# Kernel tuning notes

Measured on AMD Instinct MI355X. Metric: run time of the kernel, lower is better.

Reference implementation:

```python
import jax, jax.numpy as jnp
import numpy as np

N, WORD, R, NW, MODES = 512, 64, 4, 1, 3
EPS = 1e-6

def setup_inputs() -> dict:
    key = jax.random.key(0)
    k1, k2, k3 = jax.random.split(key, 3)
    B, T, C = 8, 16, 1024
    IFACE = R * WORD + R + NW * WORD + NW + NW * WORD + NW * WORD + R + NW + NW + R * MODES  # 471
    return {
        'controller_output': jax.random.normal(k1, (B, T, C), dtype=jnp.float32),
        'W_if': jax.random.normal(k2, (C, IFACE), dtype=jnp.float32) * 0.02,
        'b_if': jnp.zeros((IFACE,), dtype=jnp.float32),
        'memory0': jax.random.normal(k3, (B, N, WORD), dtype=jnp.float32) * 0.1,
    }

def _content_weights(keys, strengths, memory):
    # keys [B,H,W], memory [B,N,W] -> [B,H,N]
    dots = jnp.einsum('bhw,bnw->bhn', keys, memory)
    knorm = jnp.linalg.norm(keys, axis=-1, keepdims=True)          # [B,H,1]
    mnorm = jnp.linalg.norm(memory, axis=-1)                        # [B,N]
    sim = dots / (knorm * mnorm[:, None, :] + EPS)
    return jax.nn.softmax(strengths[..., None] * sim, axis=-1)

def _allocation(usage):
    # usage [B,N] -> allocation weighting [B,N] (DNC free-list)
    phi = jnp.argsort(usage, axis=-1)                               # ascending usage
    su = jnp.take_along_axis(usage, phi, axis=-1)
    cp = jnp.cumprod(jnp.concatenate([jnp.ones_like(su[:, :1]), su[:, :-1]], axis=-1), axis=-1)
    a_sorted = (1.0 - su) * cp
    inv = jnp.argsort(phi, axis=-1)
    return jnp.take_along_axis(a_sorted, inv, axis=-1)

def _parse(v, B):
    idx = [0]
    def take(n):
        out = v[:, idx[0]:idx[0] + n]; idx[0] += n; return out
    read_keys = take(R * WORD).reshape(B, R, WORD)
    read_str = jax.nn.softplus(take(R))
    write_keys = take(NW * WORD).reshape(B, NW, WORD)
    write_str = jax.nn.softplus(take(NW))
    erase = jax.nn.sigmoid(take(NW * WORD).reshape(B, NW, WORD))
    write_vec = take(NW * WORD).reshape(B, NW, WORD)
    free_g = jax.nn.sigmoid(take(R))
    alloc_g = jax.nn.sigmoid(take(NW))
    write_g = jax.nn.sigmoid(take(NW))
    modes = jax.nn.softmax(take(R * MODES).reshape(B, R, MODES), axis=-1)
    return read_keys, read_str, write_keys, write_str, erase, write_vec, free_g, alloc_g, write_g, modes

def _dnc_forward(controller_output, W_if, b_if, memory0):
    B = controller_output.shape[0]
    iface = jnp.einsum('btc,ci->bti', controller_output, W_if) + b_if   # [B,T,I]
    off_diag = 1.0 - jnp.eye(N, dtype=memory0.dtype)

    read_w0 = jnp.zeros((B, R, N), memory0.dtype)
    usage0 = jnp.zeros((B, N), memory0.dtype)
    link0 = jnp.zeros((B, N, N), memory0.dtype)
    prec0 = jnp.zeros((B, N), memory0.dtype)

    def step(carry, iface_t):
        memory, read_w, usage, link, prec = carry
        (rk, rs, wk, ws, erase, wv, fg, ag, wg, modes) = _parse(iface_t, B)
        # write content addressing on previous memory
        w_content = _content_weights(wk, ws, memory)                 # [B,NW,N]
        alloc = _allocation(usage)                                   # [B,N]
        ww = wg[..., None] * (ag[..., None] * alloc[:, None, :] + (1.0 - ag[..., None]) * w_content)  # [B,NW,N]
        # usage update
        psi = jnp.prod(1.0 - fg[..., None] * read_w, axis=1)         # [B,N]
        ws_all = 1.0 - jnp.prod(1.0 - ww, axis=1)                    # [B,N]
        usage = (usage + ws_all - usage * ws_all) * psi
        # memory erase + write
        keep = jnp.prod(1.0 - ww[:, :, :, None] * erase[:, :, None, :], axis=1)  # [B,N,W]
        add = jnp.einsum('bwn,bwk->bnk', ww, wv)
        memory = memory * keep + add
        # temporal linkage (aggregated over write heads, as in the module)
        ww_sum = jnp.sum(ww, axis=1)                                  # [B,N]
        link = ((1.0 - ww_sum[:, :, None] - ww_sum[:, None, :]) * link
                + ww_sum[:, :, None] * prec[:, None, :]) * off_diag
        prec = (1.0 - jnp.sum(ww_sum, axis=-1, keepdims=True)) * prec + ww_sum
        # read addressing on updated memory
        r_content = _content_weights(rk, rs, memory)                  # [B,R,N]
        fwd = jnp.einsum('bnm,brm->brn', link, read_w)
        bwd = jnp.einsum('bmn,brm->brn', link, read_w)
        read_w = (modes[:, :, 0:1] * bwd + modes[:, :, 1:2] * r_content + modes[:, :, 2:3] * fwd)
        read_words = jnp.einsum('brn,bnw->brw', read_w, memory)       # [B,R,W]
        return (memory, read_w, usage, link, prec), read_words

    carry0 = (memory0, read_w0, usage0, link0, prec0)
    (memory, read_w, usage, link, prec), read_words = jax.lax.scan(step, carry0, jnp.swapaxes(iface, 0, 1))
    read_words = jnp.swapaxes(read_words, 0, 1)                       # [B,T,R,W]
    return read_words

def reference(controller_output, W_if, b_if, memory0):
    return _dnc_forward(controller_output, W_if, b_if, memory0)
```

## Files before the change

### kernel.cpp

```cpp
#include <hip/hip_runtime.h>
#include <math.h>


#define NBATCH 8
#define GPB    32
#define NBLK   (NBATCH*GPB)
#define BS     512
#define NROW   16
#define NTT    16
#define NSLOT  512
#define WRD    64
#define RH     4
#define NIF    471
#define LSTR   520
#define MSTR   65
#define EPSV   1e-6f

#define B_ALO  0
#define B_WM   512
#define B_EN   1536
#define B_SEP  5632
#define B_RWP  5760
#define BATF   13952
#define IFCF   (NBATCH*NTT*NIF)
#define PARF   (NBATCH*BATF)

#define P_ERA 328
#define P_WV  392
#define P_WS  456
#define P_FG  457
#define P_AG  461
#define P_WG  462
#define P_MOD 464
#define P_WKN 476
#define P_RKN 477

__device__ __forceinline__ float sigm(float x){ return 1.f/(1.f+expf(-x)); }
__device__ __forceinline__ float softpl(float x){ return x>0.f ? x+log1pf(expf(-x)) : log1pf(expf(x)); }
__device__ __forceinline__ float red16s(float v){ v+=__shfl_xor(v,1,16); v+=__shfl_xor(v,2,16); v+=__shfl_xor(v,4,16); v+=__shfl_xor(v,8,16); return v; }
__device__ __forceinline__ float red32s(float v){ v+=__shfl_xor(v,1,32); v+=__shfl_xor(v,2,32); v+=__shfl_xor(v,4,32); v+=__shfl_xor(v,8,32); v+=__shfl_xor(v,16,32); return v; }
__device__ __forceinline__ float red32m(float v){ v*=__shfl_xor(v,1,32); v*=__shfl_xor(v,2,32); v*=__shfl_xor(v,4,32); v*=__shfl_xor(v,8,32); v*=__shfl_xor(v,16,32); return v; }
__device__ __forceinline__ float red64s(float v){
  v+=__shfl_xor(v,1); v+=__shfl_xor(v,2); v+=__shfl_xor(v,4);
  v+=__shfl_xor(v,8); v+=__shfl_xor(v,16); v+=__shfl_xor(v,32); return v; }

__device__ __forceinline__ void stg(float* p, float v){
  __hip_atomic_store(p, v, __ATOMIC_RELAXED, __HIP_MEMORY_SCOPE_AGENT);
}
__device__ __forceinline__ float ldc(const float* p){
  return __hip_atomic_load(p, __ATOMIC_RELAXED, __HIP_MEMORY_SCOPE_AGENT);
}
__device__ __forceinline__ void stg2(float* p, float x, float y){
  union { float2 f; unsigned long long u; } v; v.f=make_float2(x,y);
  __hip_atomic_store((unsigned long long*)p, v.u, __ATOMIC_RELAXED, __HIP_MEMORY_SCOPE_AGENT);
}
__device__ __forceinline__ float2 ldc2(const float* p){
  union { float2 f; unsigned long long u; } v;
  v.u=__hip_atomic_load((const unsigned long long*)p, __ATOMIC_RELAXED, __HIP_MEMORY_SCOPE_AGENT);
  return v.f;
}

__device__ __forceinline__ void lbar(unsigned* flg, int b, int g, unsigned gen, int tid){
  asm volatile("s_waitcnt vmcnt(0)" ::: "memory");
  __syncthreads();
  if (tid==0) __hip_atomic_store(flg+b*512+g*16, gen, __ATOMIC_RELAXED, __HIP_MEMORY_SCOPE_AGENT);
  if (tid<GPB){
    while (__hip_atomic_load(flg+b*512+tid*16, __ATOMIC_RELAXED, __HIP_MEMORY_SCOPE_AGENT) < gen)
      __builtin_amdgcn_s_sleep(1);
  }
  __syncthreads();
  asm volatile("" ::: "memory");
}

__global__ void __launch_bounds__(BS)
dnc_kernel(const float* __restrict__ ctrl, const float* __restrict__ wif,
           const float* __restrict__ bif, const float* __restrict__ mem0,
           float* __restrict__ out, float* __restrict__ ws, unsigned* __restrict__ flg)
{
  const int tid = threadIdx.x;
  const int bid = blockIdx.x;
  const int b   = bid & 7;
  const int g   = bid >> 3;
  const int n0  = g * NROW;

  __shared__ __align__(16) float L  [NROW*LSTR];
  __shared__ __align__(16) float LT [NROW*LSTR];
  __shared__ __align__(16) float Mem[NROW*MSTR];
  __shared__ __align__(16) float rwl[RH*NSLOT];
  __shared__ __align__(16) float wwl[NSLOT];
  __shared__ __align__(16) float usagel[NSLOT];
  __shared__ __align__(16) float precl[NSLOT];
  __shared__ __align__(16) float prs[488];
  __shared__ __align__(16) float aux[248];
  float* ern    = aux;
  float* fwdb   = aux+64;
  float* bwdb   = aux+128;
  float* modesA = aux+192;
  float* red    = aux+216;

  for (int i=tid; i<NROW*LSTR; i+=BS){ L[i]=0.f; LT[i]=0.f; }
  for (int i=tid; i<NROW*WRD; i+=BS){
    int r=i>>6, k=i&63;
    Mem[r*MSTR+k] = mem0[(size_t)(b*NSLOT + n0 + r)*WRD + k];
  }
  if (tid<NSLOT){ usagel[tid]=0.f; precl[tid]=0.f; }
  if (g < NTT){
    float* ctrlrow = rwl;
    const float* crow = ctrl + (size_t)(b*NTT+g)*1024;
    for (int i=tid;i<1024;i+=BS) ctrlrow[i]=crow[i];
    __syncthreads();
    if (tid<NIF){
      int j=tid;
      float a0=0.f,a1=0.f,a2=0.f,a3=0.f;
      const float* wp = wif + j;
      for (int c=0;c<1024;c+=4){
        a0 += ctrlrow[c+0]*wp[(size_t)(c+0)*NIF];
        a1 += ctrlrow[c+1]*wp[(size_t)(c+1)*NIF];
        a2 += ctrlrow[c+2]*wp[(size_t)(c+2)*NIF];
        a3 += ctrlrow[c+3]*wp[(size_t)(c+3)*NIF];
      }
      ws[(size_t)(b*NTT+g)*NIF + j] = ((a0+a1)+(a2+a3)) + bif[j];
    }
  }
  __syncthreads();
  for (int i=tid;i<RH*NSLOT;i+=BS) rwl[i]=0.f;

  __syncthreads();
  __builtin_amdgcn_fence(__ATOMIC_RELEASE, "agent");
  if (tid==0) __hip_atomic_store(flg+b*512+g*16, 1u, __ATOMIC_RELAXED, __HIP_MEMORY_SCOPE_AGENT);
  if (tid<GPB){
    while (__hip_atomic_load(flg+b*512+tid*16, __ATOMIC_RELAXED, __HIP_MEMORY_SCOPE_AGENT) < 1u)
      __builtin_amdgcn_s_sleep(1);
  }
  __syncthreads();
  __builtin_amdgcn_fence(__ATOMIC_ACQUIRE, "agent");

  {
    float* qb = ws + IFCF + 0*PARF + b*BATF;
    const float* ifc0 = ws + (size_t)(b*NTT+0)*NIF;
    {
      int row=tid>>5, sub=tid&31;
      float wd=0.f, ms=0.f;
      #pragma unroll
      for (int j=0;j<2;j++){
        int k=sub*2+j; float m=Mem[row*MSTR+k];
        wd += m*ifc0[260+k]; ms += m*m;
      }
      wd=red32s(wd); ms=red32s(ms);
      if (sub==0) stg2(qb+B_WM+2*(n0+row), wd, sqrtf(ms));
    }
    {
      int row=tid>>5, sub=tid&31, n=n0+row;
      float u_n=usagel[n], pr=1.f;
      for (int m=sub;m<NSLOT;m+=32){
        float um=usagel[m];
        if (um<u_n || (um==u_n && m<n)) pr*=um;
      }
      pr=red32m(pr);
      if (sub==0) stg(qb+B_ALO+n, (1.f-u_n)*pr);
    }
  }
  {
    const float* ifc = ws + (size_t)(b*NTT+0)*NIF;
    if (tid<324) prs[tid]=ifc[tid];
    __syncthreads();
    if (tid<4) prs[256+tid]=softpl(prs[256+tid]);
    else if (tid==4) prs[P_WS]=softpl(ifc[324]);
    else if (tid>=8 && tid<12) prs[P_FG+(tid-8)]=sigm(ifc[453+(tid-8)]);
    else if (tid==12) prs[P_AG]=sigm(ifc[457]);
    else if (tid==13) prs[P_WG]=sigm(ifc[458]);
    else if (tid>=16 && tid<20){
      int r=tid-16;
      float x0=ifc[459+r*3],x1=ifc[460+r*3],x2=ifc[461+r*3];
      float mx=fmaxf(x0,fmaxf(x1,x2));
      float e0=expf(x0-mx),e1=expf(x1-mx),e2=expf(x2-mx),s=e0+e1+e2;
      prs[P_MOD+r*3+0]=e0/s; prs[P_MOD+r*3+1]=e1/s; prs[P_MOD+r*3+2]=e2/s;
      modesA[r*3+0]=e0/s; modesA[r*3+1]=e1/s; modesA[r*3+2]=e2/s;
    }
    else if (tid>=64 && tid<128) prs[P_ERA+(tid-64)]=sigm(ifc[325+(tid-64)]);
    else if (tid>=192 && tid<256) prs[P_WV+(tid-192)]=ifc[389+(tid-192)];
    {
      int wv=tid>>6, lane=tid&63;
      if (wv<4){
        float v = (wv==0)? prs[260+lane] : prs[(wv-1)*64+lane];
        v = red64s(v*v);
        if (lane==0) prs[P_WKN+wv]=sqrtf(v);
        if (wv==0){
          float u=prs[192+lane];
          u=red64s(u*u);
          if (lane==0) prs[480]=sqrtf(u);
        }
      }
    }
  }
  lbar(flg, b, g, 2u, tid);

  for (int t=0; t<=NTT; t++){
    const float* pb = ws + IFCF + (t&1)*PARF + b*BATF;
    float*       qb = ws + IFCF + ((t+1)&1)*PARF + b*BATF;
    float* mprev = modesA + 12*((t+1)&1);
    float* mcur  = modesA + 12*(t&1);
    const int row = tid>>5, sub = tid&31;

    float2 en[4]; float2 sep2=make_float2(1.f,1.f); float rwpv=0.f;
    float2 wm=make_float2(0.f,1.f); float al=0.f;
    float2 wk2=make_float2(0.f,0.f);
    if (t>0){
      #pragma unroll
      for (int i=0;i<4;i++) en[i]=ldc2(pb+B_EN+2*(tid+BS*i));
      if (tid<64){ int gp=tid>>1, c=tid&1; sep2=ldc2(pb+B_SEP+gp*4+c*2); }
      if (t>=2 && tid<256) rwpv=ldc(pb+B_RWP+(tid&31)*256+g*8+(tid>>5));
    }
    if (t<NTT){
      wm=ldc2(pb+B_WM+2*tid);
      al=ldc(pb+B_ALO+tid);
    }
    if (t<NTT-1){
      const float* ifn = ws + (size_t)(b*NTT+(t+1))*NIF;
      wk2 = *(const float2*)(ifn+260+sub*2);
    }

    float ewv=0.f;
    if (t<NTT){
      ewv=expf(prs[P_WS]*wm.x/(prs[P_WKN]*wm.y+EPSV));
      wwl[tid]=ewv;
    }
    if (t>0 && tid<64){
      float vx=sep2.x, vy=sep2.y;
      vx+=__shfl_xor(vx,2); vy+=__shfl_xor(vy,2);
      vx+=__shfl_xor(vx,4); vy+=__shfl_xor(vy,4);
      vx+=__shfl_xor(vx,8); vy+=__shfl_xor(vy,8);
      vx+=__shfl_xor(vx,16); vy+=__shfl_xor(vy,16);
      vx+=__shfl_xor(vx,32); vy+=__shfl_xor(vy,32);
      if (tid<2){ red[tid*2]=vx; red[tid*2+1]=vy; }
    }
    __syncthreads();

    float psi=1.f;
    if (t>0){
      float rwv[4];
      #pragma unroll
      for (int i=0;i<4;i++){
        rwv[i] = en[i].y + mprev[i*3+1]*en[i].x/red[i];
        rwl[i*NSLOT+tid] = rwv[i];
      }
      psi=(1.f-prs[P_FG+0]*rwv[0])*(1.f-prs[P_FG+1]*rwv[1])
         *(1.f-prs[P_FG+2]*rwv[2])*(1.f-prs[P_FG+3]*rwv[3]);
    }
    if (t<NTT){ float v=red64s(ewv); if ((tid&63)==0) red[4+(tid>>6)]=v; }
    __syncthreads();

    if (t>0 && tid<256){
      int r=tid>>6, k=tid&63;
      float a=0.f;
      #pragma unroll
      for (int rr=0;rr<4;rr++){
        float4 rv=*(const float4*)&rwl[r*NSLOT+n0+rr*4];
        a += rv.x*Mem[(rr*4+0)*MSTR+k] + rv.y*Mem[(rr*4+1)*MSTR+k]
           + rv.z*Mem[(rr*4+2)*MSTR+k] + rv.w*Mem[(rr*4+3)*MSTR+k];
      }
      stg(qb+B_RWP+g*256+tid, a);
    }
    if (t>=2 && tid<256){
      float s=red32s(rwpv);
      if ((tid&31)==0) out[(size_t)(b*NTT+(t-2))*256 + g*8 + (tid>>5)] = s;
    }
    if (t==NTT) break;
    float wwv;
    {
      const float Sw=red[4]+red[5]+red[6]+red[7]+red[8]+red[9]+red[10]+red[11];
      wwv=prs[P_WG]*(prs[P_AG]*al+(1.f-prs[P_AG])*ewv/Sw);
      wwl[tid]=wwv;
      usagel[tid]=(usagel[tid]+wwv-usagel[tid]*wwv)*psi;
      float v=red64s(wwv);
      if ((tid&63)==0) red[12+(tid>>6)]=v;
    }
    __syncthreads();

    {
      float wn =wwl[n0+row];
      float pmn=precl[n0+row];
      float* Lr = &L[row*LSTR];
      float* Tr = &LT[row*LSTR];
      float fa0=0.f,fa1=0.f,fa2=0.f,fa3=0.f, ba0=0.f,ba1=0.f,ba2=0.f,ba3=0.f;
      #pragma unroll 2
      for (int jj=0;jj<4;jj++){
        int mb=(sub+32*jj)*4;
        float4 wm4=*(float4*)&wwl[mb];
        float4 pm4=*(float4*)&precl[mb];
        float c0=1.f-wn-wm4.x, c1=1.f-wn-wm4.y, c2=1.f-wn-wm4.z, c3=1.f-wn-wm4.w;
        int d=(n0+row)-mb;
        float4 l4=*(float4*)&Lr[mb];
        l4.x=c0*l4.x+wn*pm4.x; l4.y=c1*l4.y+wn*pm4.y;
        l4.z=c2*l4.z+wn*pm4.z; l4.w=c3*l4.w+wn*pm4.w;
        if (d>=0 && d<4) ((float*)&l4)[d]=0.f;
        *(float4*)&Lr[mb]=l4;
        float4 r0=*(const float4*)&rwl[0*NSLOT+mb];
        float4 r1=*(const float4*)&rwl[1*NSLOT+mb];
        float4 r2=*(const float4*)&rwl[2*NSLOT+mb];
        float4 r3=*(const float4*)&rwl[3*NSLOT+mb];
        fa0+=l4.x*r0.x+l4.y*r0.y+l4.z*r0.z+l4.w*r0.w;
        fa1+=l4.x*r1.x+l4.y*r1.y+l4.z*r1.z+l4.w*r1.w;
        fa2+=l4.x*r2.x+l4.y*r2.y+l4.z*r2.z+l4.w*r2.w;
        fa3+=l4.x*r3.x+l4.y*r3.y+l4.z*r3.z+l4.w*r3.w;
        float4 t4=*(float4*)&Tr[mb];
        t4.x=c0*t4.x+wm4.x*pmn; t4.y=c1*t4.y+wm4.y*pmn;
        t4.z=c2*t4.z+wm4.z*pmn; t4.w=c3*t4.w+wm4.w*pmn;
        if (d>=0 && d<4) ((float*)&t4)[d]=0.f;
        *(float4*)&Tr[mb]=t4;
        ba0+=t4.x*r0.x+t4.y*r0.y+t4.z*r0.z+t4.w*r0.w;
        ba1+=t4.x*r1.x+t4.y*r1.y+t4.z*r1.z+t4.w*r1.w;
        ba2+=t4.x*r2.x+t4.y*r2.y+t4.z*r2.z+t4.w*r2.w;
        ba3+=t4.x*r3.x+t4.y*r3.y+t4.z*r3.z+t4.w*r3.w;
      }
      fa0=red32s(fa0); fa1=red32s(fa1); fa2=red32s(fa2); fa3=red32s(fa3);
      ba0=red32s(ba0); ba1=red32s(ba1); ba2=red32s(ba2); ba3=red32s(ba3);
      if (sub==0){
        fwdb[0*NROW+row]=fa0; fwdb[1*NROW+row]=fa1; fwdb[2*NROW+row]=fa2; fwdb[3*NROW+row]=fa3;
        bwdb[0*NROW+row]=ba0; bwdb[1*NROW+row]=ba1; bwdb[2*NROW+row]=ba2; bwdb[3*NROW+row]=ba3;
      }
    }
    {
      float wn=wwl[n0+row];
      float2 er =*(float2*)&prs[P_ERA+sub*2];
      float2 wvv=*(float2*)&prs[P_WV +sub*2];
      float m0=Mem[row*MSTR+sub*2+0], m1=Mem[row*MSTR+sub*2+1];
      m0=m0*(1.f-wn*er.x)+wn*wvv.x; m1=m1*(1.f-wn*er.y)+wn*wvv.y;
      Mem[row*MSTR+sub*2+0]=m0; Mem[row*MSTR+sub*2+1]=m1;
      float2 k0=*(float2*)&prs[  0+sub*2];
      float2 k1=*(float2*)&prs[ 64+sub*2];
      float2 k2=*(float2*)&prs[128+sub*2];
      float2 k3=*(float2*)&prs[192+sub*2];
      float rd0=m0*k0.x+m1*k0.y;
      float rd1=m0*k1.x+m1*k1.y;
      float rd2=m0*k2.x+m1*k2.y;
      float rd3=m0*k3.x+m1*k3.y;
      float ms=m0*m0+m1*m1;
      float wd=m0*wk2.x+m1*wk2.y;
      rd0=red32s(rd0); rd1=red32s(rd1); rd2=red32s(rd2); rd3=red32s(rd3);
      ms=red32s(ms); wd=red32s(wd);
      if (sub==0){
        float mn=sqrtf(ms);
        ern[0*NROW+row]=expf(prs[256]*rd0/(prs[P_RKN+0]*mn+EPSV));
        ern[1*NROW+row]=expf(prs[257]*rd1/(prs[P_RKN+1]*mn+EPSV));
        ern[2*NROW+row]=expf(prs[258]*rd2/(prs[P_RKN+2]*mn+EPSV));
        ern[3*NROW+row]=expf(prs[259]*rd3/(prs[480]*mn+EPSV));
        stg2(qb+B_WM+2*(n0+row), wd, mn);
      }
    }
    {
      int n=n0+row;
      float u_n=usagel[n], pr=1.f;
      #pragma unroll
      for (int mb=0; mb<4; mb++){
        int m0=(sub+32*mb)*4;
        float4 u4=*(const float4*)&usagel[m0];
        pr *= (u4.x<u_n || (u4.x==u_n && m0  <n)) ? u4.x : 1.f;
        pr *= (u4.y<u_n || (u4.y==u_n && m0+1<n)) ? u4.y : 1.f;
        pr *= (u4.z<u_n || (u4.z==u_n && m0+2<n)) ? u4.z : 1.f;
        pr *= (u4.w<u_n || (u4.w==u_n && m0+3<n)) ? u4.w : 1.f;
      }
      pr=red32m(pr);
      if (sub==0) stg(qb+B_ALO+n, (1.f-u_n)*pr);
    }
    __syncthreads();

    {
      const float Sww=red[12]+red[13]+red[14]+red[15]+red[16]+red[17]+red[18]+red[19];
      precl[tid]=(1.f-Sww)*precl[tid]+wwl[tid];
    }
    if (tid<64){
      int r=tid>>4, rw_=tid&15;
      float e=ern[r*NROW+rw_];
      float nn=mcur[r*3+0]*bwdb[r*NROW+rw_] + mcur[r*3+2]*fwdb[r*NROW+rw_];
      stg2(qb+B_EN+2*(r*NSLOT+n0+rw_), e, nn);
      float v=e;
      v+=__shfl_xor(v,1,16); v+=__shfl_xor(v,2,16);
      v+=__shfl_xor(v,4,16); v+=__shfl_xor(v,8,16);
      if (rw_==0) stg(qb+B_SEP+g*4+r, v);
    }

    asm volatile("s_waitcnt vmcnt(0)" ::: "memory");
    __syncthreads();
    if (tid==0) __hip_atomic_store(flg+b*512+g*16, 3u+(unsigned)t, __ATOMIC_RELAXED, __HIP_MEMORY_SCOPE_AGENT);

    if (t<NTT-1){
      const float* ifc = ws + (size_t)(b*NTT+(t+1))*NIF;
      float* mnx = modesA + 12*((t+1)&1);
      if (tid<324) prs[tid]=ifc[tid];
      __syncthreads();
      if (tid<4) prs[256+tid]=softpl(prs[256+tid]);
      else if (tid==4) prs[P_WS]=softpl(ifc[324]);
      else if (tid>=8 && tid<12) prs[P_FG+(tid-8)]=sigm(ifc[453+(tid-8)]);
      else if (tid==12) prs[P_AG]=sigm(ifc[457]);
      else if (tid==13) prs[P_WG]=sigm(ifc[458]);
      else if (tid>=16 && tid<20){
        int r=tid-16;
        float x0=ifc[459+r*3],x1=ifc[460+r*3],x2=ifc[461+r*3];
        float mx=fmaxf(x0,fmaxf(x1,x2));
        float e0=expf(x0-mx),e1=expf(x1-mx),e2=expf(x2-mx),s=e0+e1+e2;
        prs[P_MOD+r*3+0]=e0/s; prs[P_MOD+r*3+1]=e1/s; prs[P_MOD+r*3+2]=e2/s;
        mnx[r*3+0]=e0/s; mnx[r*3+1]=e1/s; mnx[r*3+2]=e2/s;
      }
      else if (tid>=64 && tid<128) prs[P_ERA+(tid-64)]=sigm(ifc[325+(tid-64)]);
      else if (tid>=192 && tid<256) prs[P_WV+(tid-192)]=ifc[389+(tid-192)];
      {
        int wv=tid>>6, lane=tid&63;
        if (wv<4){
          float v = (wv==0)? prs[260+lane] : prs[(wv-1)*64+lane];
          v = red64s(v*v);
          if (lane==0) prs[P_WKN+wv]=sqrtf(v);
          if (wv==0){
            float u=prs[192+lane];
            u=red64s(u*u);
            if (lane==0) prs[480]=sqrtf(u);
          }
        }
      }
    }

    if (tid<GPB){
      while (__hip_atomic_load(flg+b*512+tid*16, __ATOMIC_RELAXED, __HIP_MEMORY_SCOPE_AGENT) < 3u+(unsigned)t)
        __builtin_amdgcn_s_sleep(1);
    }
    __syncthreads();
    asm volatile("" ::: "memory");
  }

  lbar(flg, b, g, 3u+NTT, tid);
  if (tid<256){
    const float* fb = ws + IFCF + ((NTT+1)&1)*PARF + b*BATF;
    float v=ldc(fb+B_RWP+(tid&31)*256+g*8+(tid>>5));
    v=red32s(v);
    if ((tid&31)==0) out[(size_t)(b*NTT+(NTT-1))*256 + g*8 + (tid>>5)] = v;
  }
}

extern "C" void kernel_launch(void* const* d_in, const int* in_sizes, int n_in,
                              void* d_out, int out_size, void* d_ws, size_t ws_size,
                              hipStream_t stream)
{
  const float* ctrl=(const float*)d_in[0];
  const float* wif =(const float*)d_in[1];
  const float* bif =(const float*)d_in[2];
  const float* mem0=(const float*)d_in[3];
  float* outp=(float*)d_out;
  unsigned* flg=(unsigned*)d_ws;
  float* wsf=(float*)((char*)d_ws+32768);

  hipMemsetAsync(d_ws, 0, 32768, stream);

  void* args[]={(void*)&ctrl,(void*)&wif,(void*)&bif,(void*)&mem0,(void*)&outp,(void*)&wsf,(void*)&flg};
  hipError_t err = hipLaunchCooperativeKernel((void*)dnc_kernel, dim3(NBLK), dim3(BS), args, 0, stream);
  if (err != hipSuccess){
    hipLaunchKernelGGL(dnc_kernel, dim3(NBLK), dim3(BS), 0, stream,
                       ctrl, wif, bif, mem0, outp, wsf, flg);
  }
}
```

Measured before the change: 267.6 us.

## Double block size to 1024 threads with one thread per memory word

Raises the block size from 512 to 1024 threads so each 16-row group gets a full 64-lane wavefront per row. Per-row reductions become 64-wide. Per-slot work is gated to the first 512 threads, and the delayed read-word reduction and output moves to threads 512-767 so it overlaps other work. This cuts per-thread serial work in the link, memory and allocation loops. In exchange it adds more barrier participants, more idle lanes in the slot phases, and higher register pressure at 1024 threads per block.

```diff
diff --git a/kernel.cpp b/kernel.cpp
--- a/kernel.cpp
+++ b/kernel.cpp
@@ -5,7 +5,7 @@
 #define NBATCH 8
 #define GPB    32
 #define NBLK   (NBATCH*GPB)
-#define BS     512
+#define BS     1024
 #define NROW   16
 #define NTT    16
 #define NSLOT  512
@@ -39,10 +39,12 @@
 __device__ __forceinline__ float softpl(float x){ return x>0.f ? x+log1pf(expf(-x)) : log1pf(expf(x)); }
 __device__ __forceinline__ float red16s(float v){ v+=__shfl_xor(v,1,16); v+=__shfl_xor(v,2,16); v+=__shfl_xor(v,4,16); v+=__shfl_xor(v,8,16); return v; }
 __device__ __forceinline__ float red32s(float v){ v+=__shfl_xor(v,1,32); v+=__shfl_xor(v,2,32); v+=__shfl_xor(v,4,32); v+=__shfl_xor(v,8,32); v+=__shfl_xor(v,16,32); return v; }
-__device__ __forceinline__ float red32m(float v){ v*=__shfl_xor(v,1,32); v*=__shfl_xor(v,2,32); v*=__shfl_xor(v,4,32); v*=__shfl_xor(v,8,32); v*=__shfl_xor(v,16,32); return v; }
 __device__ __forceinline__ float red64s(float v){
   v+=__shfl_xor(v,1); v+=__shfl_xor(v,2); v+=__shfl_xor(v,4);
   v+=__shfl_xor(v,8); v+=__shfl_xor(v,16); v+=__shfl_xor(v,32); return v; }
+__device__ __forceinline__ float red64m(float v){
+  v*=__shfl_xor(v,1); v*=__shfl_xor(v,2); v*=__shfl_xor(v,4);
+  v*=__shfl_xor(v,8); v*=__shfl_xor(v,16); v*=__shfl_xor(v,32); return v; }
 
 __device__ __forceinline__ void stg(float* p, float v){
   __hip_atomic_store(p, v, __ATOMIC_RELAXED, __HIP_MEMORY_SCOPE_AGENT);
@@ -99,8 +101,8 @@
   float* red    = aux+216;
 
   for (int i=tid; i<NROW*LSTR; i+=BS){ L[i]=0.f; LT[i]=0.f; }
-  for (int i=tid; i<NROW*WRD; i+=BS){
-    int r=i>>6, k=i&63;
+  {
+    int r=tid>>6, k=tid&63;
     Mem[r*MSTR+k] = mem0[(size_t)(b*NSLOT + n0 + r)*WRD + k];
   }
   if (tid<NSLOT){ usagel[tid]=0.f; precl[tid]=0.f; }
@@ -138,25 +140,26 @@
   {
     float* qb = ws + IFCF + 0*PARF + b*BATF;
     const float* ifc0 = ws + (size_t)(b*NTT+0)*NIF;
-    {
-      int row=tid>>5, sub=tid&31;
-      float wd=0.f, ms=0.f;
-      #pragma unroll
-      for (int j=0;j<2;j++){
-        int k=sub*2+j; float m=Mem[row*MSTR+k];
-        wd += m*ifc0[260+k]; ms += m*m;
-      }
-      wd=red32s(wd); ms=red32s(ms);
+    int row=tid>>6, sub=tid&63;
+    {
+      float m=Mem[row*MSTR+sub];
+      float wd=m*ifc0[260+sub], ms=m*m;
+      wd=red64s(wd); ms=red64s(ms);
       if (sub==0) stg2(qb+B_WM+2*(n0+row), wd, sqrtf(ms));
     }
     {
-      int row=tid>>5, sub=tid&31, n=n0+row;
+      int n=n0+row;
       float u_n=usagel[n], pr=1.f;
-      for (int m=sub;m<NSLOT;m+=32){
-        float um=usagel[m];
-        if (um<u_n || (um==u_n && m<n)) pr*=um;
-      }
-      pr=red32m(pr);
+      #pragma unroll
+      for (int mb=0; mb<2; mb++){
+        int m0=(sub+64*mb)*4;
+        float4 u4=*(const float4*)&usagel[m0];
+        pr *= (u4.x<u_n || (u4.x==u_n && m0  <n)) ? u4.x : 1.f;
+        pr *= (u4.y<u_n || (u4.y==u_n && m0+1<n)) ? u4.y : 1.f;
+        pr *= (u4.z<u_n || (u4.z==u_n && m0+2<n)) ? u4.z : 1.f;
+        pr *= (u4.w<u_n || (u4.w==u_n && m0+3<n)) ? u4.w : 1.f;
+      }
+      pr=red64m(pr);
       if (sub==0) stg(qb+B_ALO+n, (1.f-u_n)*pr);
     }
   }
@@ -200,30 +203,34 @@
     float*       qb = ws + IFCF + ((t+1)&1)*PARF + b*BATF;
     float* mprev = modesA + 12*((t+1)&1);
     float* mcur  = modesA + 12*(t&1);
-    const int row = tid>>5, sub = tid&31;
+    const int row = tid>>6, sub = tid&63;
 
     float2 en[4]; float2 sep2=make_float2(1.f,1.f); float rwpv=0.f;
-    float2 wm=make_float2(0.f,1.f); float al=0.f;
-    float2 wk2=make_float2(0.f,0.f);
-    if (t>0){
-      #pragma unroll
-      for (int i=0;i<4;i++) en[i]=ldc2(pb+B_EN+2*(tid+BS*i));
-      if (tid<64){ int gp=tid>>1, c=tid&1; sep2=ldc2(pb+B_SEP+gp*4+c*2); }
-      if (t>=2 && tid<256) rwpv=ldc(pb+B_RWP+(tid&31)*256+g*8+(tid>>5));
-    }
-    if (t<NTT){
+    float2 wm=make_float2(0.f,1.f); float al=0.f; float wkv=0.f;
+    if (t>0 && tid<512){
+      #pragma unroll
+      for (int i=0;i<4;i++) en[i]=ldc2(pb+B_EN+2*(tid+512*i));
+    }
+    if (t>0 && tid<64){ int gp=tid>>1, c=tid&1; sep2=ldc2(pb+B_SEP+gp*4+c*2); }
+    if (t>=2 && tid>=512 && tid<768){
+      int q=tid-512;
+      rwpv=ldc(pb+B_RWP+(q&31)*256+g*8+(q>>5));
+    }
+    if (t<NTT && tid<512){
       wm=ldc2(pb+B_WM+2*tid);
       al=ldc(pb+B_ALO+tid);
     }
     if (t<NTT-1){
       const float* ifn = ws + (size_t)(b*NTT+(t+1))*NIF;
-      wk2 = *(const float2*)(ifn+260+sub*2);
+      wkv = ifn[260+sub];
     }
 
     float ewv=0.f;
-    if (t<NTT){
+    if (t<NTT && tid<512){
       ewv=expf(prs[P_WS]*wm.x/(prs[P_WKN]*wm.y+EPSV));
       wwl[tid]=ewv;
+      float v=red64s(ewv);
+      if ((tid&63)==0) red[4+(tid>>6)]=v;
     }
     if (t>0 && tid<64){
       float vx=sep2.x, vy=sep2.y;
@@ -237,7 +244,7 @@
     __syncthreads();
 
     float psi=1.f;
-    if (t>0){
+    if (t>0 && tid<512){
       float rwv[4];
       #pragma unroll
       for (int i=0;i<4;i++){
@@ -247,7 +254,6 @@
       psi=(1.f-prs[P_FG+0]*rwv[0])*(1.f-prs[P_FG+1]*rwv[1])
          *(1.f-prs[P_FG+2]*rwv[2])*(1.f-prs[P_FG+3]*rwv[3]);
     }
-    if (t<NTT){ float v=red64s(ewv); if ((tid&63)==0) red[4+(tid>>6)]=v; }
     __syncthreads();
 
     if (t>0 && tid<256){
@@ -261,19 +267,21 @@
       }
       stg(qb+B_RWP+g*256+tid, a);
     }
-    if (t>=2 && tid<256){
+    if (t>=2 && tid>=512 && tid<768){
+      int q=tid-512;
       float s=red32s(rwpv);
-      if ((tid&31)==0) out[(size_t)(b*NTT+(t-2))*256 + g*8 + (tid>>5)] = s;
+      if ((q&31)==0) out[(size_t)(b*NTT+(t-2))*256 + g*8 + (q>>5)] = s;
     }
     if (t==NTT) break;
-    float wwv;
-    {
-      const float Sw=red[4]+red[5]+red[6]+red[7]+red[8]+red[9]+red[10]+red[11];
-      wwv=prs[P_WG]*(prs[P_AG]*al+(1.f-prs[P_AG])*ewv/Sw);
-      wwl[tid]=wwv;
-      usagel[tid]=(usagel[tid]+wwv-usagel[tid]*wwv)*psi;
-      float v=red64s(wwv);
-      if ((tid&63)==0) red[12+(tid>>6)]=v;
+    {
+      if (tid<512){
+        const float Sw=red[4]+red[5]+red[6]+red[7]+red[8]+red[9]+red[10]+red[11];
+        float wwv=prs[P_WG]*(prs[P_AG]*al+(1.f-prs[P_AG])*ewv/Sw);
+        wwl[tid]=wwv;
+        usagel[tid]=(usagel[tid]+wwv-usagel[tid]*wwv)*psi;
+        float v=red64s(wwv);
+        if ((tid&63)==0) red[12+(tid>>6)]=v;
+      }
     }
     __syncthreads();
 
@@ -283,9 +291,9 @@
       float* Lr = &L[row*LSTR];
       float* Tr = &LT[row*LSTR];
       float fa0=0.f,fa1=0.f,fa2=0.f,fa3=0.f, ba0=0.f,ba1=0.f,ba2=0.f,ba3=0.f;
-      #pragma unroll 2
-      for (int jj=0;jj<4;jj++){
-        int mb=(sub+32*jj)*4;
+      #pragma unroll
+      for (int jj=0;jj<2;jj++){
+        int mb=(sub+64*jj)*4;
         float4 wm4=*(float4*)&wwl[mb];
         float4 pm4=*(float4*)&precl[mb];
         float c0=1.f-wn-wm4.x, c1=1.f-wn-wm4.y, c2=1.f-wn-wm4.z, c3=1.f-wn-wm4.w;
@@ -313,8 +321,8 @@
         ba2+=t4.x*r2.x+t4.y*r2.y+t4.z*r2.z+t4.w*r2.w;
         ba3+=t4.x*r3.x+t4.y*r3.y+t4.z*r3.z+t4.w*r3.w;
       }
-      fa0=red32s(fa0); fa1=red32s(fa1); fa2=red32s(fa2); fa3=red32s(fa3);
-      ba0=red32s(ba0); ba1=red32s(ba1); ba2=red32s(ba2); ba3=red32s(ba3);
+      fa0=red64s(fa0); fa1=red64s(fa1); fa2=red64s(fa2); fa3=red64s(fa3);
+      ba0=red64s(ba0); ba1=red64s(ba1); ba2=red64s(ba2); ba3=red64s(ba3);
       if (sub==0){
         fwdb[0*NROW+row]=fa0; fwdb[1*NROW+row]=fa1; fwdb[2*NROW+row]=fa2; fwdb[3*NROW+row]=fa3;
         bwdb[0*NROW+row]=ba0; bwdb[1*NROW+row]=ba1; bwdb[2*NROW+row]=ba2; bwdb[3*NROW+row]=ba3;
@@ -322,23 +330,16 @@
     }
     {
       float wn=wwl[n0+row];
-      float2 er =*(float2*)&prs[P_ERA+sub*2];
-      float2 wvv=*(float2*)&prs[P_WV +sub*2];
-      float m0=Mem[row*MSTR+sub*2+0], m1=Mem[row*MSTR+sub*2+1];
-      m0=m0*(1.f-wn*er.x)+wn*wvv.x; m1=m1*(1.f-wn*er.y)+wn*wvv.y;
-      Mem[row*MSTR+sub*2+0]=m0; Mem[row*MSTR+sub*2+1]=m1;
-      float2 k0=*(float2*)&prs[  0+sub*2];
-      float2 k1=*(float2*)&prs[ 64+sub*2];
-      float2 k2=*(float2*)&prs[128+sub*2];
-      float2 k3=*(float2*)&prs[192+sub*2];
-      float rd0=m0*k0.x+m1*k0.y;
-      float rd1=m0*k1.x+m1*k1.y;
-      float rd2=m0*k2.x+m1*k2.y;
-      float rd3=m0*k3.x+m1*k3.y;
-      float ms=m0*m0+m1*m1;
-      float wd=m0*wk2.x+m1*wk2.y;
-      rd0=red32s(rd0); rd1=red32s(rd1); rd2=red32s(rd2); rd3=red32s(rd3);
-      ms=red32s(ms); wd=red32s(wd);
+      float m=Mem[row*MSTR+sub];
+      m = m*(1.f-wn*prs[P_ERA+sub]) + wn*prs[P_WV+sub];
+      Mem[row*MSTR+sub]=m;
+      float rd0=m*prs[  0+sub];
+      float rd1=m*prs[ 64+sub];
+      float rd2=m*prs[128+sub];
+      float rd3=m*prs[192+sub];
+      float ms=m*m, wd=m*wkv;
+      rd0=red64s(rd0); rd1=red64s(rd1); rd2=red64s(rd2); rd3=red64s(rd3);
+      ms=red64s(ms); wd=red64s(wd);
       if (sub==0){
         float mn=sqrtf(ms);
         ern[0*NROW+row]=expf(prs[256]*rd0/(prs[P_RKN+0]*mn+EPSV));
@@ -352,20 +353,20 @@
       int n=n0+row;
       float u_n=usagel[n], pr=1.f;
       #pragma unroll
-      for (int mb=0; mb<4; mb++){
-        int m0=(sub+32*mb)*4;
+      for (int mb=0; mb<2; mb++){
+        int m0=(sub+64*mb)*4;
         float4 u4=*(const float4*)&usagel[m0];
         pr *= (u4.x<u_n || (u4.x==u_n && m0  <n)) ? u4.x : 1.f;
         pr *= (u4.y<u_n || (u4.y==u_n && m0+1<n)) ? u4.y : 1.f;
         pr *= (u4.z<u_n || (u4.z==u_n && m0+2<n)) ? u4.z : 1.f;
         pr *= (u4.w<u_n || (u4.w==u_n && m0+3<n)) ? u4.w : 1.f;
       }
-      pr=red32m(pr);
+      pr=red64m(pr);
       if (sub==0) stg(qb+B_ALO+n, (1.f-u_n)*pr);
     }
     __syncthreads();
 
-    {
+    if (tid<512){
       const float Sww=red[12]+red[13]+red[14]+red[15]+red[16]+red[17]+red[18]+red[19];
       precl[tid]=(1.f-Sww)*precl[tid]+wwl[tid];
     }
@@ -374,9 +375,7 @@
       float e=ern[r*NROW+rw_];
       float nn=mcur[r*3+0]*bwdb[r*NROW+rw_] + mcur[r*3+2]*fwdb[r*NROW+rw_];
       stg2(qb+B_EN+2*(r*NSLOT+n0+rw_), e, nn);
-      float v=e;
-      v+=__shfl_xor(v,1,16); v+=__shfl_xor(v,2,16);
-      v+=__shfl_xor(v,4,16); v+=__shfl_xor(v,8,16);
+      float v=red16s(e);
       if (rw_==0) stg(qb+B_SEP+g*4+r, v);
     }
 
```

New measurement: 350.6 us. 1.31x slower.
